# Performance work log

Hardware: AMD Instinct MI355X
Metric: run time of the kernel (lower is better)

## Reference

```python
import jax, jax.numpy as jnp
import numpy as np

V = 50257   # vocab
P = 2048    # max positions
D = 768     # hidden
H = 12      # heads
F = 3072    # 4*D ffn
NL = 12     # layers
L = 2048    # seq len
EPS = 1e-5


def setup_inputs() -> dict:
    key = jax.random.key(0)
    ks = jax.random.split(key, 12)
    r = lambda k, shp: jax.random.normal(k, shp, jnp.float32) * 0.02
    return dict(
        input_ids=jax.random.randint(ks[0], (1, L), 0, V, dtype=jnp.int32),
        attention_mask=jnp.ones((1, L), jnp.int32),
        wte=r(ks[1], (V, D)),
        wpe=r(ks[2], (P, D)),
        lnf_w=jnp.ones((D,), jnp.float32),
        lnf_b=jnp.zeros((D,), jnp.float32),
        ln1_w=jnp.ones((NL, D), jnp.float32),
        ln1_b=jnp.zeros((NL, D), jnp.float32),
        qw=r(ks[3], (NL, D, D)),
        kw=r(ks[4], (NL, D, D)),
        vw=r(ks[5], (NL, D, D)),
        ow=r(ks[6], (NL, D, D)),
        ob=jnp.zeros((NL, D), jnp.float32),
        ln2_w=jnp.ones((NL, D), jnp.float32),
        ln2_b=jnp.zeros((NL, D), jnp.float32),
        fcw=r(ks[7], (NL, D, F)),
        fcb=jnp.zeros((NL, F), jnp.float32),
        pw=r(ks[8], (NL, F, D)),
        pb=jnp.zeros((NL, D), jnp.float32),
    )


def _ln(x, w, b):
    mu = jnp.mean(x, -1, keepdims=True)
    var = jnp.mean((x - mu) ** 2, -1, keepdims=True)
    return (x - mu) * jax.lax.rsqrt(var + EPS) * w + b


def reference(input_ids, attention_mask, wte, wpe, lnf_w, lnf_b,
              ln1_w, ln1_b, qw, kw, vw, ow, ob, ln2_w, ln2_b,
              fcw, fcb, pw, pb):
    ids = input_ids.reshape(-1, input_ids.shape[-1])          # [1, L]
    pos = jnp.cumsum(attention_mask, -1) - 1
    pos = jnp.where(attention_mask == 0, 1, pos)
    h = (wte[ids] + wpe[pos])[0]                               # [L, D]

    key_valid = attention_mask[0] > 0                          # actual_length mask
    mask = jnp.tril(jnp.ones((L, L), bool)) & key_valid[None, :]  # causal+pad
    dh = D // H

    def layer(h, p):
        l1w, l1b, Wq, Wk, Wv, Wo, bo, l2w, l2b, Wf, bf, Wp, bp = p
        x = _ln(h, l1w, l1b)
        q = (x @ Wq).reshape(L, H, dh)
        k = (x @ Wk).reshape(L, H, dh)
        v = (x @ Wv).reshape(L, H, dh)
        # GPT-Neo attention: NO 1/sqrt(dh) scaling
        scores = jnp.einsum('qhd,khd->hqk', q, k)
        scores = jnp.where(mask[None], scores, jnp.float32(-1e9))
        attn = jax.nn.softmax(scores, axis=-1)
        ctx = jnp.einsum('hqk,khd->qhd', attn, v).reshape(L, D)
        h = h + ctx @ Wo + bo
        y = _ln(h, l2w, l2b)
        h = h + jax.nn.gelu(y @ Wf + bf, approximate=True) @ Wp + bp
        return h, None

    h, _ = jax.lax.scan(layer, h, (ln1_w, ln1_b, qw, kw, vw, ow, ob,
                                   ln2_w, ln2_b, fcw, fcb, pw, pb))
    return _ln(h[None, :, :], lnf_w, lnf_b)                    # [1, L, D]
```

## Files before the change

### kernel.cpp

```cpp
#include <hip/hip_runtime.h>
#include <hip/hip_bf16.h>
#include <math.h>
#include <stdint.h>

#define L 2048
#define D 768
#define H 12
#define DH 64
#define F 3072
#define NL 12
#define QKVN 2304

typedef __attribute__((ext_vector_type(8))) short bf16x8;
typedef __attribute__((ext_vector_type(4))) float f32x4;

__device__ __forceinline__ ushort f2bf(float x) {
    union { float f; uint32_t u; } c; c.f = x;
    uint32_t r = c.u + 0x7FFFu + ((c.u >> 16) & 1u);
    return (ushort)(r >> 16);
}

__device__ __forceinline__ uint32_t cvt_pk_bf16(float lo, float hi) {
    uint32_t r;
    asm("v_cvt_pk_bf16_f32 %0, %1, %2" : "=v"(r) : "v"(lo), "v"(hi));
    return r;
}

__device__ __forceinline__ float ex2(float x) {
    float r;
    asm("v_exp_f32 %0, %1" : "=v"(r) : "v"(x));
    return r;
}

#define LOG2E 1.4426950408889634f

__device__ __forceinline__ bf16x8 ldfrag(const ushort* p) {
    ushort4 lo = *(const ushort4*)(p);
    ushort4 hi = *(const ushort4*)(p + 16);
    bf16x8 f;
    f[0] = (short)lo.x; f[1] = (short)lo.y; f[2] = (short)lo.z; f[3] = (short)lo.w;
    f[4] = (short)hi.x; f[5] = (short)hi.y; f[6] = (short)hi.z; f[7] = (short)hi.w;
    return f;
}

__device__ __forceinline__ float gelu_tanh(float x) {
    float c = 0.7978845608028654f;
    float u = c * (x + 0.044715f * x * x * x);
    u = fminf(fmaxf(u, -10.f), 10.f);
    float t = ex2(u * (2.0f * LOG2E));
    float th = (t - 1.0f) / (t + 1.0f);
    return 0.5f * x * (1.0f + th);
}

__global__ void pos_kernel(const int* __restrict__ mask, int* __restrict__ pos) {
    __shared__ int sm[L];
    for (int i = threadIdx.x; i < L; i += blockDim.x) sm[i] = mask[i];
    __syncthreads();
    int t = blockIdx.x * blockDim.x + threadIdx.x;
    if (t < L) {
        int s = 0;
        for (int j = 0; j <= t; ++j) s += sm[j];
        int p = s - 1;
        if (sm[t] == 0) p = 1;
        pos[t] = p;
    }
}

__global__ void maskb_kernel(const int* __restrict__ mask, float* __restrict__ mb) {
    int i = blockIdx.x * blockDim.x + threadIdx.x;
    if (i < L) mb[i] = mask[i] ? 0.f : -2.0e9f;
}

__global__ __launch_bounds__(256) void embed_kernel(const int* __restrict__ ids,
                                                    const int* __restrict__ pos,
                                                    const float* __restrict__ wte,
                                                    const float* __restrict__ wpe,
                                                    float* __restrict__ h) {
    int t = blockIdx.x;
    int id = ids[t];
    int p = pos[t];
    const float* we = wte + (size_t)id * D;
    const float* wp = wpe + (size_t)p * D;
    float* hr = h + (size_t)t * D;
#pragma unroll
    for (int i = 0; i < 3; ++i) {
        int d = threadIdx.x + i * 256;
        hr[d] = we[d] + wp[d];
    }
}

template <bool OUTBF>
__global__ __launch_bounds__(256) void ln_kernel(const float* __restrict__ in,
                                                 const float* __restrict__ w,
                                                 const float* __restrict__ b,
                                                 float* __restrict__ outF,
                                                 ushort* __restrict__ outB) {
    __shared__ float red[2][4];
    int row = blockIdx.x;
    const float* x = in + (size_t)row * D;
    int t = threadIdx.x;
    float v0 = x[t], v1 = x[t + 256], v2 = x[t + 512];
    float s = v0 + v1 + v2;
    float ss = v0 * v0 + v1 * v1 + v2 * v2;
#pragma unroll
    for (int o = 32; o; o >>= 1) {
        s += __shfl_xor(s, o);
        ss += __shfl_xor(ss, o);
    }
    int wave = t >> 6;
    if ((t & 63) == 0) { red[0][wave] = s; red[1][wave] = ss; }
    __syncthreads();
    s = red[0][0] + red[0][1] + red[0][2] + red[0][3];
    ss = red[1][0] + red[1][1] + red[1][2] + red[1][3];
    float mean = s * (1.f / D);
    float var = ss * (1.f / D) - mean * mean;
    float rstd = rsqrtf(var + 1e-5f);
#pragma unroll
    for (int i = 0; i < 3; ++i) {
        int d = t + i * 256;
        float vv = (i == 0) ? v0 : (i == 1) ? v1 : v2;
        float y = (vv - mean) * rstd * w[d] + b[d];
        if (OUTBF) outB[(size_t)row * D + d] = f2bf(y);
        else       outF[(size_t)row * D + d] = y;
    }
}

template <int S, bool OUTBF>
__global__ __launch_bounds__(256) void redln_kernel(const float* __restrict__ part,
                                                    const float* __restrict__ bias,
                                                    float* __restrict__ h,
                                                    const float* __restrict__ lnw,
                                                    const float* __restrict__ lnb,
                                                    ushort* __restrict__ outB,
                                                    float* __restrict__ outF) {
    __shared__ float red[2][4];
    int row = blockIdx.x;
    int t = threadIdx.x;
    float v[3];
    float s = 0.f, ss = 0.f;
#pragma unroll
    for (int i = 0; i < 3; ++i) {
        int d = t + i * 256;
        float x = h[(size_t)row * D + d] + bias[d];
#pragma unroll
        for (int sp = 0; sp < S; ++sp)
            x += part[((size_t)sp * L + row) * D + d];
        v[i] = x;
        h[(size_t)row * D + d] = x;
        s += x;
        ss += x * x;
    }
#pragma unroll
    for (int o = 32; o; o >>= 1) {
        s += __shfl_xor(s, o);
        ss += __shfl_xor(ss, o);
    }
    int wave = t >> 6;
    if ((t & 63) == 0) { red[0][wave] = s; red[1][wave] = ss; }
    __syncthreads();
    s = red[0][0] + red[0][1] + red[0][2] + red[0][3];
    ss = red[1][0] + red[1][1] + red[1][2] + red[1][3];
    float mean = s * (1.f / D);
    float var = ss * (1.f / D) - mean * mean;
    float rstd = rsqrtf(var + 1e-5f);
#pragma unroll
    for (int i = 0; i < 3; ++i) {
        int d = t + i * 256;
        float y = (v[i] - mean) * rstd * lnw[d] + lnb[d];
        if (OUTBF) outB[(size_t)row * D + d] = f2bf(y);
        else       outF[(size_t)row * D + d] = y;
    }
}

__global__ __launch_bounds__(256) void tcast_f32(const float* __restrict__ in,
                                                 ushort* __restrict__ out,
                                                 int K, int N,
                                                 size_t inStride, size_t outStride) {
    in += blockIdx.z * inStride;
    out += blockIdx.z * outStride;
    __shared__ float tile[64][65];
    int k0 = blockIdx.y * 64, n0 = blockIdx.x * 64;
    int t = threadIdx.x;
    int cl = t & 63, rg = t >> 6;
#pragma unroll
    for (int i = 0; i < 16; ++i) {
        int r = rg + 4 * i;
        tile[r][cl] = in[(size_t)(k0 + r) * N + n0 + cl];
    }
    __syncthreads();
#pragma unroll
    for (int i = 0; i < 16; ++i) {
        int r = rg + 4 * i;
        out[(size_t)(n0 + r) * K + k0 + cl] = f2bf(tile[cl][r]);
    }
}

template <int ACT, bool OUTBF, int SPLITK, bool VSPLIT>
__global__ __launch_bounds__(256) void gemm_bf16(const ushort* __restrict__ A,
                                                 const ushort* __restrict__ Bt,
                                                 const float* __restrict__ bias,
                                                 const float* __restrict__ resid,
                                                 float* __restrict__ outF,
                                                 ushort* __restrict__ outB,
                                                 float* __restrict__ pout,
                                                 ushort* __restrict__ vTout,
                                                 int M, int N, int K) {
    __shared__ __align__(16) char lds[65536];
    const int tid = threadIdx.x;
    const int lane = tid & 63, w = tid >> 6;
    const int wr = w >> 1, wc = w & 1;
    const int bm = blockIdx.y * 128, bn = blockIdx.x * 128;
    const int l15 = lane & 15, l4 = lane >> 4;
    const int kLen = K / SPLITK;
    const int kStart = (SPLITK > 1) ? blockIdx.z * kLen : 0;

    const int srow = tid >> 1, hf = tid & 1;
    const int swz = (srow & 7) << 4;
    const int rb = srow * 128;
    int offlo[4], offhi[4];
#pragma unroll
    for (int cc = 0; cc < 4; ++cc) {
        int blo = (cc & 1) * 32 + ((cc >> 1) & 1) * 8 + hf * 64;
        offlo[cc] = rb + ((blo & 0x70) ^ swz) + (blo & 15);
        int bhi = blo + 16;
        offhi[cc] = rb + ((bhi & 0x70) ^ swz) + (bhi & 15);
    }
    const int fxor = (l15 & 7) << 4;

    f32x4 acc[4][4];
#pragma unroll
    for (int m = 0; m < 4; ++m)
#pragma unroll
        for (int n = 0; n < 4; ++n)
            acc[m][n] = (f32x4){0.f, 0.f, 0.f, 0.f};

    const ushort* Ag = A + (size_t)(bm + srow) * K + kStart + hf * 32;
    const ushort* Bg = Bt + (size_t)(bn + srow) * K + kStart + hf * 32;

    uint4 ax[4], bx[4];
#pragma unroll
    for (int cc = 0; cc < 4; ++cc) {
        ax[cc] = *(const uint4*)(Ag + cc * 8);
        bx[cc] = *(const uint4*)(Bg + cc * 8);
    }

    for (int k0 = 0; k0 < kLen; k0 += 64) {
        char* Ab = lds + ((k0 >> 6) & 1) * 32768;
        char* Bb = Ab + 16384;
        {
            uint2 t0, t1;
#pragma unroll
            for (int cc = 0; cc < 4; ++cc) {
                t0.x = ax[cc].x; t0.y = ax[cc].y; t1.x = ax[cc].z; t1.y = ax[cc].w;
                *(uint2*)(Ab + offlo[cc]) = t0;
                *(uint2*)(Ab + offhi[cc]) = t1;
                t0.x = bx[cc].x; t0.y = bx[cc].y; t1.x = bx[cc].z; t1.y = bx[cc].w;
                *(uint2*)(Bb + offlo[cc]) = t0;
                *(uint2*)(Bb + offhi[cc]) = t1;
            }
        }
        __syncthreads();
        if (k0 + 64 < kLen) {
#pragma unroll
            for (int cc = 0; cc < 4; ++cc) {
                ax[cc] = *(const uint4*)(Ag + k0 + 64 + cc * 8);
                bx[cc] = *(const uint4*)(Bg + k0 + 64 + cc * 8);
            }
        }
        bf16x8 af[4][2], bfv[4][2];
#pragma unroll
        for (int m = 0; m < 4; ++m)
#pragma unroll
            for (int ks = 0; ks < 2; ++ks)
                af[m][ks] = *(const bf16x8*)(Ab + (wr * 64 + m * 16 + l15) * 128 +
                                             ((ks * 64 + l4 * 16) ^ fxor));
#pragma unroll
        for (int n = 0; n < 4; ++n)
#pragma unroll
            for (int ks = 0; ks < 2; ++ks)
                bfv[n][ks] = *(const bf16x8*)(Bb + (wc * 64 + n * 16 + l15) * 128 +
                                              ((ks * 64 + l4 * 16) ^ fxor));
#pragma unroll
        for (int m = 0; m < 4; ++m)
#pragma unroll
            for (int n = 0; n < 4; ++n) {
                acc[m][n] = __builtin_amdgcn_mfma_f32_16x16x32_bf16(
                    af[m][0], bfv[n][0], acc[m][n], 0, 0, 0);
                acc[m][n] = __builtin_amdgcn_mfma_f32_16x16x32_bf16(
                    af[m][1], bfv[n][1], acc[m][n], 0, 0, 0);
            }
    }

    if (SPLITK > 1) {
        const size_t sb = (size_t)blockIdx.z * M;
#pragma unroll
        for (int m = 0; m < 4; ++m)
#pragma unroll
            for (int n = 0; n < 4; ++n) {
                int col = bn + wc * 64 + n * 16 + l15;
#pragma unroll
                for (int r = 0; r < 4; ++r) {
                    int row = bm + wr * 64 + m * 16 + l4 * 4 + r;
                    pout[(sb + row) * N + col] = acc[m][n][r];
                }
            }
    } else {
#pragma unroll
        for (int m = 0; m < 4; ++m)
#pragma unroll
            for (int n = 0; n < 4; ++n) {
                int col = bn + wc * 64 + n * 16 + l15;
                int row0 = bm + wr * 64 + m * 16 + l4 * 4;
                if (VSPLIT && col >= 2 * D) {
                    union { ushort4 s; uint32_t d[2]; } pk;
                    pk.d[0] = cvt_pk_bf16(acc[m][n][0], acc[m][n][1]);
                    pk.d[1] = cvt_pk_bf16(acc[m][n][2], acc[m][n][3]);
                    *(ushort4*)(vTout + (size_t)(col - 2 * D) * L + row0) = pk.s;
                } else {
#pragma unroll
                    for (int r = 0; r < 4; ++r) {
                        int row = row0 + r;
                        float v = acc[m][n][r];
                        if (bias) v += bias[col];
                        if (ACT == 1) v = gelu_tanh(v);
                        if (resid) v += resid[(size_t)row * N + col];
                        if (OUTBF) outB[(size_t)row * N + col] = f2bf(v);
                        else       outF[(size_t)row * N + col] = v;
                    }
                }
            }
    }
}

template <int NS>
__global__ __launch_bounds__(256) void attn_kernel(const ushort* __restrict__ qkv,
                                                   const ushort* __restrict__ vT,
                                                   const float* __restrict__ maskb,
                                                   float* __restrict__ po,
                                                   float* __restrict__ pm,
                                                   float* __restrict__ pl) {
    __shared__ __align__(16) char Kl[2][8192];
    __shared__ __align__(16) char Vl[2][8192];
    __shared__ float Ml[2][64];
    const int hh = blockIdx.y;
    const int sp = blockIdx.z;
    const int q0 = ((int)gridDim.x - 1 - (int)blockIdx.x) * 64;
    const int tid = threadIdx.x;
    const int lane = tid & 63, w = tid >> 6;
    const int l15 = lane & 15, l4 = lane >> 4;
    const int qg = q0 + w * 16 + l15;
    const int qmin = q0 + w * 16;

    const int nt = q0 / 64 + 1;
    const int chunk = (nt + NS - 1) / NS;
    const int it0 = sp * chunk;
    int it1 = it0 + chunk;
    if (it1 > nt) it1 = nt;

    f32x4 o[4];
#pragma unroll
    for (int i = 0; i < 4; ++i) o[i] = (f32x4){0.f, 0.f, 0.f, 0.f};
    float mrun = -1e30f, lrun = 0.f;

    if (it0 < it1) {
        bf16x8 qf[2];
#pragma unroll
        for (int ks = 0; ks < 2; ++ks)
            qf[ks] = ldfrag(qkv + (size_t)qg * QKVN + hh * 64 + ks * 32 + l4 * 4);

        const int srow = tid >> 2, c = tid & 3;
        const int blo = (c & 1) * 32 + (c >> 1) * 8;
        const int swz = (srow & 7) << 4;
        const int rb = srow * 128;
        const int lo4 = blo & 15;
        const int s0 = rb + (((blo)      & 0x70) ^ swz) + lo4;
        const int s1 = rb + (((blo + 16) & 0x70) ^ swz) + lo4;
        const int s2 = rb + (((blo + 64) & 0x70) ^ swz) + lo4;
        const int s3 = rb + (((blo + 80) & 0x70) ^ swz) + lo4;
        const int fxor = (l15 & 7) << 4;

        const ushort* Ksrc = qkv + (size_t)srow * QKVN + D + hh * 64 + c * 8;
        const ushort* Vsrc = vT + (size_t)(hh * 64 + srow) * L + c * 8;

        uint4 ka, kb, va, vb;
        float mv = 0.f;
        {
            const size_t koff = (size_t)(it0 * 64) * QKVN;
            ka = *(const uint4*)(Ksrc + koff);
            kb = *(const uint4*)(Ksrc + koff + 32);
            va = *(const uint4*)(Vsrc + it0 * 64);
            vb = *(const uint4*)(Vsrc + it0 * 64 + 32);
            if (tid < 64) mv = maskb[it0 * 64 + tid];
        }

        for (int it = it0; it < it1; ++it) {
            const int kv0 = it * 64;
            const int b = it & 1;
            {
                char* Kb = Kl[b];
                char* Vb = Vl[b];
                uint2 t0, t1;
                t0.x = ka.x; t0.y = ka.y; t1.x = ka.z; t1.y = ka.w;
                *(uint2*)(Kb + s0) = t0;
                *(uint2*)(Kb + s1) = t1;
                t0.x = kb.x; t0.y = kb.y; t1.x = kb.z; t1.y = kb.w;
                *(uint2*)(Kb + s2) = t0;
                *(uint2*)(Kb + s3) = t1;
                t0.x = va.x; t0.y = va.y; t1.x = va.z; t1.y = va.w;
                *(uint2*)(Vb + s0) = t0;
                *(uint2*)(Vb + s1) = t1;
                t0.x = vb.x; t0.y = vb.y; t1.x = vb.z; t1.y = vb.w;
                *(uint2*)(Vb + s2) = t0;
                *(uint2*)(Vb + s3) = t1;
                if (tid < 64) Ml[b][tid] = mv;
            }
            __syncthreads();
            if (it + 1 < it1) {
                const size_t koff = (size_t)(kv0 + 64) * QKVN;
                ka = *(const uint4*)(Ksrc + koff);
                kb = *(const uint4*)(Ksrc + koff + 32);
                va = *(const uint4*)(Vsrc + kv0 + 64);
                vb = *(const uint4*)(Vsrc + kv0 + 96);
                if (tid < 64) mv = maskb[kv0 + 64 + tid];
            }

            const char* Kb = Kl[b];
            const char* Vb = Vl[b];

            f32x4 st[4];
#pragma unroll
            for (int m = 0; m < 4; ++m) st[m] = (f32x4){0.f, 0.f, 0.f, 0.f};
            __builtin_amdgcn_s_setprio(1);
#pragma unroll
            for (int m = 0; m < 4; ++m)
#pragma unroll
                for (int ks = 0; ks < 2; ++ks) {
                    bf16x8 kf = *(const bf16x8*)(Kb + (m * 16 + l15) * 128 +
                                                 ((ks * 64 + l4 * 16) ^ fxor));
                    st[m] = __builtin_amdgcn_mfma_f32_16x16x32_bf16(kf, qf[ks], st[m], 0, 0, 0);
                }
            __builtin_amdgcn_s_setprio(0);

            float p[4][4];
            float tmax = -1e30f;
            const bool full = (kv0 + 63 <= qmin);
            if (full) {
#pragma unroll
                for (int m = 0; m < 4; ++m)
#pragma unroll
                    for (int r = 0; r < 4; ++r) {
                        int kl = m * 16 + l4 * 4 + r;
                        float s = fmaf(st[m][r], LOG2E, Ml[b][kl]);
                        p[m][r] = s;
                        tmax = fmaxf(tmax, s);
                    }
            } else {
#pragma unroll
                for (int m = 0; m < 4; ++m)
#pragma unroll
                    for (int r = 0; r < 4; ++r) {
                        int kl = m * 16 + l4 * 4 + r;
                        float s = fmaf(st[m][r], LOG2E, Ml[b][kl]);
                        if (kv0 + kl > qg) s = -1e30f;
                        p[m][r] = s;
                        tmax = fmaxf(tmax, s);
                    }
            }
            tmax = fmaxf(tmax, __shfl_xor(tmax, 16));
            tmax = fmaxf(tmax, __shfl_xor(tmax, 32));
            const bool noresc = __all(tmax <= mrun);
            float mnew = noresc ? mrun : fmaxf(mrun, tmax);
            float scale = noresc ? 1.f : ex2(mrun - mnew);
            float ts = 0.f;
#pragma unroll
            for (int m = 0; m < 4; ++m)
#pragma unroll
                for (int r = 0; r < 4; ++r) {
                    float e = ex2(p[m][r] - mnew);
                    p[m][r] = e;
                    ts += e;
                }
            ts += __shfl_xor(ts, 16);
            ts += __shfl_xor(ts, 32);
            lrun = lrun * scale + ts;
            mrun = mnew;

            bf16x8 pf[2];
#pragma unroll
            for (int g = 0; g < 2; ++g) {
                union { bf16x8 v; uint32_t d[4]; } pu;
                pu.d[0] = cvt_pk_bf16(p[2 * g][0], p[2 * g][1]);
                pu.d[1] = cvt_pk_bf16(p[2 * g][2], p[2 * g][3]);
                pu.d[2] = cvt_pk_bf16(p[2 * g + 1][0], p[2 * g + 1][1]);
                pu.d[3] = cvt_pk_bf16(p[2 * g + 1][2], p[2 * g + 1][3]);
                pf[g] = pu.v;
            }
            if (!noresc) {
#pragma unroll
                for (int i = 0; i < 4; ++i) {
                    o[i][0] *= scale; o[i][1] *= scale; o[i][2] *= scale; o[i][3] *= scale;
                }
            }
            __builtin_amdgcn_s_setprio(1);
#pragma unroll
            for (int dhb = 0; dhb < 4; ++dhb)
#pragma unroll
                for (int g = 0; g < 2; ++g) {
                    bf16x8 vf = *(const bf16x8*)(Vb + (dhb * 16 + l15) * 128 +
                                                 ((g * 64 + l4 * 16) ^ fxor));
                    o[dhb] = __builtin_amdgcn_mfma_f32_16x16x32_bf16(vf, pf[g], o[dhb], 0, 0, 0);
                }
            __builtin_amdgcn_s_setprio(0);
        }
    }

    const size_t pb = (size_t)(sp * H + hh) * L + qg;
    if (l4 == 0) { pm[pb] = mrun; pl[pb] = lrun; }
    float* op = po + pb * 64;
#pragma unroll
    for (int dhb = 0; dhb < 4; ++dhb)
        *(f32x4*)(op + dhb * 16 + l4 * 4) = o[dhb];
}

template <int NS>
__global__ __launch_bounds__(256) void attn_combine(const float* __restrict__ po,
                                                    const float* __restrict__ pm,
                                                    const float* __restrict__ pl,
                                                    ushort* __restrict__ ctx) {
    const int hh = blockIdx.y;
    const int q = blockIdx.x * 64 + (threadIdx.x >> 2);
    const int d0 = (threadIdx.x & 3) * 16;
    size_t idx[NS];
    float mm = -1e30f;
#pragma unroll
    for (int s = 0; s < NS; ++s) {
        idx[s] = (size_t)(s * H + hh) * L + q;
        mm = fmaxf(mm, pm[idx[s]]);
    }
    float e[NS];
    float l = 0.f;
#pragma unroll
    for (int s = 0; s < NS; ++s) {
        e[s] = ex2(pm[idx[s]] - mm);
        l += pl[idx[s]] * e[s];
    }
    float rinv = 1.0f / l;
    ushort* cp = ctx + (size_t)q * D + hh * 64 + d0;
#pragma unroll
    for (int j = 0; j < 16; j += 4) {
        float acc[4] = {0.f, 0.f, 0.f, 0.f};
#pragma unroll
        for (int s = 0; s < NS; ++s) {
            const float* op = po + idx[s] * 64 + d0 + j;
            float4 v = *(const float4*)op;
            acc[0] += v.x * e[s];
            acc[1] += v.y * e[s];
            acc[2] += v.z * e[s];
            acc[3] += v.w * e[s];
        }
        ushort4 pk;
        pk.x = f2bf(acc[0] * rinv);
        pk.y = f2bf(acc[1] * rinv);
        pk.z = f2bf(acc[2] * rinv);
        pk.w = f2bf(acc[3] * rinv);
        *(ushort4*)(cp + j) = pk;
    }
}

extern "C" void kernel_launch(void* const* d_in, const int* in_sizes, int n_in,
                              void* d_out, int out_size, void* d_ws, size_t ws_size,
                              hipStream_t stream) {
    const int* ids = (const int*)d_in[0];
    const int* amask = (const int*)d_in[1];
    const float* wte = (const float*)d_in[2];
    const float* wpe = (const float*)d_in[3];
    const float* lnf_w = (const float*)d_in[4];
    const float* lnf_b = (const float*)d_in[5];
    const float* ln1_w = (const float*)d_in[6];
    const float* ln1_b = (const float*)d_in[7];
    const float* qw = (const float*)d_in[8];
    const float* kw = (const float*)d_in[9];
    const float* vw = (const float*)d_in[10];
    const float* ow = (const float*)d_in[11];
    const float* ob = (const float*)d_in[12];
    const float* ln2_w = (const float*)d_in[13];
    const float* ln2_b = (const float*)d_in[14];
    const float* fcw = (const float*)d_in[15];
    const float* fcb = (const float*)d_in[16];
    const float* pw = (const float*)d_in[17];
    const float* pb = (const float*)d_in[18];

    char* p = (char*)d_ws;
    auto take = [&](size_t bytes) -> char* {
        char* r = p;
        p += (bytes + 4095) & ~(size_t)4095;
        return r;
    };
    ushort* wqkvT = (ushort*)take((size_t)NL * QKVN * D * 2);
    ushort* woT   = (ushort*)take((size_t)NL * D * D * 2);
    ushort* fcwT  = (ushort*)take((size_t)NL * F * D * 2);
    ushort* pwT   = (ushort*)take((size_t)NL * D * F * 2);
    float*  h     = (float*)take((size_t)L * D * 4);
    ushort* xb    = (ushort*)take((size_t)L * D * 2);
    ushort* qkvb  = (ushort*)take((size_t)L * QKVN * 2);
    ushort* vTb   = (ushort*)take((size_t)D * L * 2);
    ushort* ctxb  = (ushort*)take((size_t)L * D * 2);
    ushort* f1b   = (ushort*)take((size_t)L * F * 2);
    float*  pk    = (float*)take((size_t)4 * L * D * 4);
    float*  po    = (float*)take((size_t)4 * H * L * 64 * 4);
    float*  pm    = (float*)take((size_t)4 * H * L * 4);
    float*  pl    = (float*)take((size_t)4 * H * L * 4);
    float*  mb    = (float*)take(L * 4);
    int*    pos   = (int*)take(L * 4);

    pos_kernel<<<8, 256, 0, stream>>>(amask, pos);
    maskb_kernel<<<8, 256, 0, stream>>>(amask, mb);
    embed_kernel<<<L, 256, 0, stream>>>(ids, pos, wte, wpe, h);

    tcast_f32<<<dim3(12, 12, NL), 256, 0, stream>>>(qw, wqkvT, D, D,
                                                    (size_t)D * D, (size_t)QKVN * D);
    tcast_f32<<<dim3(12, 12, NL), 256, 0, stream>>>(kw, wqkvT + (size_t)D * D, D, D,
                                                    (size_t)D * D, (size_t)QKVN * D);
    tcast_f32<<<dim3(12, 12, NL), 256, 0, stream>>>(vw, wqkvT + (size_t)2 * D * D, D, D,
                                                    (size_t)D * D, (size_t)QKVN * D);
    tcast_f32<<<dim3(12, 12, NL), 256, 0, stream>>>(ow, woT, D, D,
                                                    (size_t)D * D, (size_t)D * D);
    tcast_f32<<<dim3(48, 12, NL), 256, 0, stream>>>(fcw, fcwT, D, F,
                                                    (size_t)D * F, (size_t)F * D);
    tcast_f32<<<dim3(12, 48, NL), 256, 0, stream>>>(pw, pwT, F, D,
                                                    (size_t)F * D, (size_t)D * F);

    ln_kernel<true><<<L, 256, 0, stream>>>(h, ln1_w, ln1_b, nullptr, xb);

    for (int l = 0; l < NL; ++l) {
        gemm_bf16<0, true, 1, true><<<dim3(QKVN / 128, L / 128), 256, 0, stream>>>(
            xb, wqkvT + (size_t)l * QKVN * D, nullptr, nullptr, nullptr, qkvb, nullptr,
            vTb, L, QKVN, D);
        attn_kernel<4><<<dim3(L / 64, H, 4), 256, 0, stream>>>(qkvb, vTb, mb,
                                                               po, pm, pl);
        attn_combine<4><<<dim3(L / 64, H), 256, 0, stream>>>(po, pm, pl, ctxb);
        gemm_bf16<0, true, 3, false><<<dim3(D / 128, L / 128, 3), 256, 0, stream>>>(
            ctxb, woT + (size_t)l * D * D, nullptr, nullptr, nullptr, nullptr, pk,
            nullptr, L, D, D);
        redln_kernel<3, true><<<L, 256, 0, stream>>>(
            pk, ob + l * D, h, ln2_w + l * D, ln2_b + l * D, xb, nullptr);
        gemm_bf16<1, true, 1, false><<<dim3(F / 128, L / 128), 256, 0, stream>>>(
            xb, fcwT + (size_t)l * F * D, fcb + l * F, nullptr, nullptr, f1b, nullptr,
            nullptr, L, F, D);
        gemm_bf16<0, true, 4, false><<<dim3(D / 128, L / 128, 4), 256, 0, stream>>>(
            f1b, pwT + (size_t)l * D * F, nullptr, nullptr, nullptr, nullptr, pk,
            nullptr, L, D, F);
        if (l < NL - 1) {
            redln_kernel<4, true><<<L, 256, 0, stream>>>(
                pk, pb + l * D, h, ln1_w + (l + 1) * D, ln1_b + (l + 1) * D, xb, nullptr);
        } else {
            redln_kernel<4, false><<<L, 256, 0, stream>>>(
                pk, pb + l * D, h, lnf_w, lnf_b, nullptr, (float*)d_out);
        }
    }
}
```

Before: 1.773 ms.

## Use direct global-to-LDS loads in GEMM and store attention partials as bf16

The GEMM mainloop now uses global_load_lds to copy A/B tiles straight into swizzled shared memory, instead of staging them through registers and then storing to LDS. Fragment reads are adjusted to the new swizzle pattern with two 8-byte loads each. Separately, the split-KV attention partial outputs are written as bf16 rather than fp32, which halves the traffic between the attention and combine kernels. In exchange, the partial sums lose precision, and the async LDS loads rely on the barrier for correct ordering.

```diff
diff --git a/kernel.cpp b/kernel.cpp
--- a/kernel.cpp
+++ b/kernel.cpp
@@ -20,6 +20,10 @@
     return (ushort)(r >> 16);
 }
 
+__device__ __forceinline__ float bf2f(ushort u) {
+    union { uint32_t i; float f; } c; c.i = ((uint32_t)u) << 16; return c.f;
+}
+
 __device__ __forceinline__ uint32_t cvt_pk_bf16(float lo, float hi) {
     uint32_t r;
     asm("v_cvt_pk_bf16_f32 %0, %1, %2" : "=v"(r) : "v"(lo), "v"(hi));
@@ -41,6 +45,22 @@
     f[0] = (short)lo.x; f[1] = (short)lo.y; f[2] = (short)lo.z; f[3] = (short)lo.w;
     f[4] = (short)hi.x; f[5] = (short)hi.y; f[6] = (short)hi.z; f[7] = (short)hi.w;
     return f;
+}
+
+__device__ __forceinline__ void gload16(const void* g, void* l) {
+    __builtin_amdgcn_global_load_lds(
+        (const __attribute__((address_space(1))) uint32_t*)(uintptr_t)g,
+        (__attribute__((address_space(3))) uint32_t*)(uintptr_t)l,
+        16, 0, 0);
+}
+
+__device__ __forceinline__ bf16x8 ldfragL(const char* rowp, int ks, int l4, int xr) {
+    int c1 = ks * 4 + (l4 >> 1);
+    int h = (l4 & 1) << 3;
+    union { bf16x8 v; uint2 d[2]; } u;
+    u.d[0] = *(const uint2*)(rowp + (((c1 << 4) ^ xr) | h));
+    u.d[1] = *(const uint2*)(rowp + ((((c1 + 2) << 4) ^ xr) | h));
+    return u.v;
 }
 
 __device__ __forceinline__ float gelu_tanh(float x) {
@@ -213,19 +233,21 @@
     const int l15 = lane & 15, l4 = lane >> 4;
     const int kLen = K / SPLITK;
     const int kStart = (SPLITK > 1) ? blockIdx.z * kLen : 0;
-
-    const int srow = tid >> 1, hf = tid & 1;
-    const int swz = (srow & 7) << 4;
-    const int rb = srow * 128;
-    int offlo[4], offhi[4];
-#pragma unroll
-    for (int cc = 0; cc < 4; ++cc) {
-        int blo = (cc & 1) * 32 + ((cc >> 1) & 1) * 8 + hf * 64;
-        offlo[cc] = rb + ((blo & 0x70) ^ swz) + (blo & 15);
-        int bhi = blo + 16;
-        offhi[cc] = rb + ((bhi & 0x70) ^ swz) + (bhi & 15);
-    }
-    const int fxor = (l15 & 7) << 4;
+    const int xr = (l15 & 7) << 4;
+
+    const ushort* AgL[4];
+    const ushort* BgL[4];
+    int ldsOff[4];
+#pragma unroll
+    for (int j = 0; j < 4; ++j) {
+        int seg = w * 4 + j;
+        int r = seg * 8 + (lane >> 3);
+        int s = lane & 7;
+        int c = s ^ (r & 7);
+        AgL[j] = A + (size_t)(bm + r) * K + kStart + c * 8;
+        BgL[j] = Bt + (size_t)(bn + r) * K + kStart + c * 8;
+        ldsOff[j] = seg * 1024 + lane * 16;
+    }
 
     f32x4 acc[4][4];
 #pragma unroll
@@ -234,52 +256,39 @@
         for (int n = 0; n < 4; ++n)
             acc[m][n] = (f32x4){0.f, 0.f, 0.f, 0.f};
 
-    const ushort* Ag = A + (size_t)(bm + srow) * K + kStart + hf * 32;
-    const ushort* Bg = Bt + (size_t)(bn + srow) * K + kStart + hf * 32;
-
-    uint4 ax[4], bx[4];
-#pragma unroll
-    for (int cc = 0; cc < 4; ++cc) {
-        ax[cc] = *(const uint4*)(Ag + cc * 8);
-        bx[cc] = *(const uint4*)(Bg + cc * 8);
+#pragma unroll
+    for (int j = 0; j < 4; ++j) {
+        gload16(AgL[j], lds + ldsOff[j]);
+        gload16(BgL[j], lds + 16384 + ldsOff[j]);
     }
 
     for (int k0 = 0; k0 < kLen; k0 += 64) {
         char* Ab = lds + ((k0 >> 6) & 1) * 32768;
         char* Bb = Ab + 16384;
-        {
-            uint2 t0, t1;
-#pragma unroll
-            for (int cc = 0; cc < 4; ++cc) {
-                t0.x = ax[cc].x; t0.y = ax[cc].y; t1.x = ax[cc].z; t1.y = ax[cc].w;
-                *(uint2*)(Ab + offlo[cc]) = t0;
-                *(uint2*)(Ab + offhi[cc]) = t1;
-                t0.x = bx[cc].x; t0.y = bx[cc].y; t1.x = bx[cc].z; t1.y = bx[cc].w;
-                *(uint2*)(Bb + offlo[cc]) = t0;
-                *(uint2*)(Bb + offhi[cc]) = t1;
-            }
-        }
         __syncthreads();
         if (k0 + 64 < kLen) {
-#pragma unroll
-            for (int cc = 0; cc < 4; ++cc) {
-                ax[cc] = *(const uint4*)(Ag + k0 + 64 + cc * 8);
-                bx[cc] = *(const uint4*)(Bg + k0 + 64 + cc * 8);
+            char* An = lds + (((k0 >> 6) + 1) & 1) * 32768;
+#pragma unroll
+            for (int j = 0; j < 4; ++j) {
+                gload16(AgL[j] + k0 + 64, An + ldsOff[j]);
+                gload16(BgL[j] + k0 + 64, An + 16384 + ldsOff[j]);
             }
         }
         bf16x8 af[4][2], bfv[4][2];
 #pragma unroll
-        for (int m = 0; m < 4; ++m)
+        for (int m = 0; m < 4; ++m) {
+            const char* rowp = Ab + (wr * 64 + m * 16 + l15) * 128;
 #pragma unroll
             for (int ks = 0; ks < 2; ++ks)
-                af[m][ks] = *(const bf16x8*)(Ab + (wr * 64 + m * 16 + l15) * 128 +
-                                             ((ks * 64 + l4 * 16) ^ fxor));
-#pragma unroll
-        for (int n = 0; n < 4; ++n)
+                af[m][ks] = ldfragL(rowp, ks, l4, xr);
+        }
+#pragma unroll
+        for (int n = 0; n < 4; ++n) {
+            const char* rowp = Bb + (wc * 64 + n * 16 + l15) * 128;
 #pragma unroll
             for (int ks = 0; ks < 2; ++ks)
-                bfv[n][ks] = *(const bf16x8*)(Bb + (wc * 64 + n * 16 + l15) * 128 +
-                                              ((ks * 64 + l4 * 16) ^ fxor));
+                bfv[n][ks] = ldfragL(rowp, ks, l4, xr);
+        }
 #pragma unroll
         for (int m = 0; m < 4; ++m)
 #pragma unroll
@@ -336,7 +345,7 @@
 __global__ __launch_bounds__(256) void attn_kernel(const ushort* __restrict__ qkv,
                                                    const ushort* __restrict__ vT,
                                                    const float* __restrict__ maskb,
-                                                   float* __restrict__ po,
+                                                   ushort* __restrict__ po,
                                                    float* __restrict__ pm,
                                                    float* __restrict__ pl) {
     __shared__ __align__(16) char Kl[2][8192];
@@ -516,14 +525,18 @@
 
     const size_t pb = (size_t)(sp * H + hh) * L + qg;
     if (l4 == 0) { pm[pb] = mrun; pl[pb] = lrun; }
-    float* op = po + pb * 64;
-#pragma unroll
-    for (int dhb = 0; dhb < 4; ++dhb)
-        *(f32x4*)(op + dhb * 16 + l4 * 4) = o[dhb];
+    ushort* op = po + pb * 64;
+#pragma unroll
+    for (int dhb = 0; dhb < 4; ++dhb) {
+        union { ushort4 s; uint32_t d[2]; } pk4;
+        pk4.d[0] = cvt_pk_bf16(o[dhb][0], o[dhb][1]);
+        pk4.d[1] = cvt_pk_bf16(o[dhb][2], o[dhb][3]);
+        *(ushort4*)(op + dhb * 16 + l4 * 4) = pk4.s;
+    }
 }
 
 template <int NS>
-__global__ __launch_bounds__(256) void attn_combine(const float* __restrict__ po,
+__global__ __launch_bounds__(256) void attn_combine(const ushort* __restrict__ po,
                                                     const float* __restrict__ pm,
                                                     const float* __restrict__ pl,
                                                     ushort* __restrict__ ctx) {
@@ -551,12 +564,11 @@
         float acc[4] = {0.f, 0.f, 0.f, 0.f};
 #pragma unroll
         for (int s = 0; s < NS; ++s) {
-            const float* op = po + idx[s] * 64 + d0 + j;
-            float4 v = *(const float4*)op;
-            acc[0] += v.x * e[s];
-            acc[1] += v.y * e[s];
-            acc[2] += v.z * e[s];
-            acc[3] += v.w * e[s];
+            ushort4 v = *(const ushort4*)(po + idx[s] * 64 + d0 + j);
+            acc[0] += bf2f(v.x) * e[s];
+            acc[1] += bf2f(v.y) * e[s];
+            acc[2] += bf2f(v.z) * e[s];
+            acc[3] += bf2f(v.w) * e[s];
         }
         ushort4 pk;
         pk.x = f2bf(acc[0] * rinv);
@@ -607,7 +619,7 @@
     ushort* ctxb  = (ushort*)take((size_t)L * D * 2);
     ushort* f1b   = (ushort*)take((size_t)L * F * 2);
     float*  pk    = (float*)take((size_t)4 * L * D * 4);
-    float*  po    = (float*)take((size_t)4 * H * L * 64 * 4);
+    ushort* po    = (ushort*)take((size_t)4 * H * L * 64 * 2);
     float*  pm    = (float*)take((size_t)4 * H * L * 4);
     float*  pl    = (float*)take((size_t)4 * H * L * 4);
     float*  mb    = (float*)take(L * 4);
```

Result: slower. 1.894 ms (+6.8%).
